# Kernel optimization log

Hardware: AMD Instinct MI355X
Metric: run time of the kernel (lower is better)

Reference implementation:

```python
import jax, jax.numpy as jnp
import numpy as np

B, SQ, SK = 2, 2048, 2048
QDIM = KDIM = HID = 1024
H = 16
DH = HID // H  # inner_dim = 64


def setup_inputs() -> dict:
    key = jax.random.key(0)
    ks = jax.random.split(key, 8)
    q = jax.random.normal(ks[0], (B, SQ, QDIM), dtype=jnp.float32)
    k = jax.random.normal(ks[1], (B, SK, KDIM), dtype=jnp.float32)
    v = jax.random.normal(ks[2], (B, SK, KDIM), dtype=jnp.float32)
    mask = jax.random.randint(ks[3], (B, SQ, SK), 0, 2).astype(jnp.bool_)
    scale = 1.0 / np.sqrt(QDIM)
    # per-head projections, stored stacked: [H, in_dim, DH]
    Wq = jax.random.normal(ks[4], (H, QDIM, DH), dtype=jnp.float32) * scale
    Wk = jax.random.normal(ks[5], (H, KDIM, DH), dtype=jnp.float32) * scale
    Wv = jax.random.normal(ks[6], (H, KDIM, DH), dtype=jnp.float32) * scale
    Wo = jax.random.normal(ks[7], (HID, QDIM), dtype=jnp.float32) * scale
    return {"q": q, "k": k, "v": v, "mask": mask,
            "Wq": Wq, "Wk": Wk, "Wv": Wv, "Wo": Wo}


def reference(q, k, v, mask, Wq, Wk, Wv, Wo):
    dh = Wq.shape[-1]
    qh = jnp.einsum('bsd,hde->bhse', q, Wq)   # [B,H,SQ,DH]
    kh = jnp.einsum('bsd,hde->bhse', k, Wk)   # [B,H,SK,DH]
    vh = jnp.einsum('bsd,hde->bhse', v, Wv)   # [B,H,SK,DH]
    scores = jnp.einsum('bhqd,bhkd->bhqk', qh, kh) / jnp.sqrt(jnp.asarray(dh, qh.dtype))
    scores = jnp.where(mask[:, None, :, :], -jnp.inf, scores)
    attn = jax.nn.softmax(scores, axis=-1)
    att = jnp.einsum('bhqk,bhkd->bhqd', attn, vh)        # [B,H,SQ,DH]
    concat = att.transpose(0, 2, 1, 3).reshape(q.shape[0], q.shape[1], -1)  # head-order concat
    return concat @ Wo  # [B,SQ,QDIM]
```

## Files before the change

### kernel.cpp

```cpp
#include <hip/hip_runtime.h>

#define NB 2
#define NH 16
#define SEQ 2048
#define DMODEL 1024
#define DHEAD 64
#define QSCALE 0.18033688f

typedef __attribute__((ext_vector_type(8))) short bf16x8;
typedef __attribute__((ext_vector_type(4))) short bf16x4;
typedef __attribute__((ext_vector_type(4))) float f32x4;
typedef __attribute__((ext_vector_type(16))) float f32x16;
typedef __attribute__((ext_vector_type(4))) int i32x4;

static __device__ __forceinline__ unsigned short f2bf(float f) {
    unsigned int u = __float_as_uint(f);
    u += 0x7fffu + ((u >> 16) & 1u);
    return (unsigned short)(u >> 16);
}
static __device__ __forceinline__ unsigned int pk2(float lo, float hi) {
    return (unsigned int)f2bf(lo) | ((unsigned int)f2bf(hi) << 16);
}
static __device__ __forceinline__ void gld_lds16(const unsigned short* g, unsigned short* l) {
    __builtin_amdgcn_global_load_lds(
        (const __attribute__((address_space(1))) unsigned int*)g,
        (__attribute__((address_space(3))) unsigned int*)l, 16, 0, 0);
}

__global__ __launch_bounds__(256) void prep_kernel(
    const int* __restrict__ mask, unsigned long long* __restrict__ mpack,
    const float* __restrict__ Wq, const float* __restrict__ Wk, const float* __restrict__ Wv,
    unsigned short* __restrict__ Wqt, unsigned short* __restrict__ Wkt,
    unsigned short* __restrict__ Wvt,
    const float* __restrict__ Wo, unsigned short* __restrict__ Wot)
{
    __shared__ __align__(16) float Ls[64][65];
    const int bid = blockIdx.x, t = threadIdx.x;

    if (bid < 1024) {
        const int wave = bid * 4 + (t >> 6);
        const int lane = t & 63;
        const int* row = mask + (size_t)wave * SEQ;
        unsigned long long* orow = mpack + (size_t)wave * (SEQ / 64);
        for (int w = 0; w < SEQ / 64; ++w) {
            int m = row[w * 64 + lane];
            unsigned long long bits = __ballot(m != 0);
            if (lane == 0) orow[w] = bits;
        }
    } else {
        const float* S; unsigned short* D; float scale; int R, tile_r, tile_c, ostride;
        if (bid < 1792) {
            const int local = bid - 1024, z = local >> 4, sel = z >> 4, h = z & 15;
            S = (sel == 0 ? Wq : sel == 1 ? Wk : Wv) + (size_t)h * DMODEL * DHEAD;
            D = (sel == 0 ? Wqt : sel == 1 ? Wkt : Wvt) + (size_t)h * DMODEL * DHEAD;
            scale = (sel == 0) ? QSCALE : 1.0f;
            tile_r = (local & 15) * 64; tile_c = 0; R = DHEAD; ostride = DMODEL;
        } else {
            const int local = bid - 1792;
            S = Wo; D = Wot; scale = 1.0f;
            tile_c = (local & 15) * 64; tile_r = (local >> 4) * 64; R = DMODEL; ostride = DMODEL;
        }
        const int c4 = (t & 15) * 4;
        for (int rr = t >> 4; rr < 64; rr += 16) {
            float4 x = *(const float4*)(S + (size_t)(tile_r + rr) * R + tile_c + c4);
            Ls[rr][c4 + 0] = x.x; Ls[rr][c4 + 1] = x.y;
            Ls[rr][c4 + 2] = x.z; Ls[rr][c4 + 3] = x.w;
        }
        __syncthreads();
        const int r4 = (t & 15) * 4;
        for (int cc = t >> 4; cc < 64; cc += 16) {
            ushort4 o;
            o.x = f2bf(Ls[r4 + 0][cc] * scale); o.y = f2bf(Ls[r4 + 1][cc] * scale);
            o.z = f2bf(Ls[r4 + 2][cc] * scale); o.w = f2bf(Ls[r4 + 3][cc] * scale);
            *(ushort4*)(D + (size_t)(tile_c + cc) * ostride + tile_r + r4) = o;
        }
    }
}

__global__ __launch_bounds__(256) void proj_gemm_kernel(
    const float* __restrict__ qf32, const float* __restrict__ kf32,
    const float* __restrict__ vf32,
    const unsigned short* __restrict__ Wqt, const unsigned short* __restrict__ Wkt,
    const unsigned short* __restrict__ Wvt,
    unsigned short* __restrict__ qh, unsigned short* __restrict__ kh,
    unsigned short* __restrict__ vt)
{
    const int bid = blockIdx.x;
    const int sx = bid >> 3;
    const int mtg = (bid & 7) * 12 + (sx >> 3);
    const int z = mtg >> 5;
    const int m0 = (mtg & 31) * 128;
    const int n0 = (sx & 7) * 128;

    const float* Af = (z == 0) ? qf32 : (z == 1) ? kf32 : vf32;
    const unsigned short* Bt = (z == 0) ? Wqt : (z == 1) ? Wkt : Wvt;

    const int t = threadIdx.x, lane = t & 63, w = t >> 6;
    const int lg = lane >> 4, ln = lane & 15;
    const int wx = w & 1, wy = w >> 1;

    __shared__ __align__(16) unsigned short SM[32768];

    int an[4], ac[4];
    #pragma unroll
    for (int i = 0; i < 4; ++i) {
        const int s = i * 256 + t;
        an[i] = s >> 3;
        ac[i] = (s & 7) ^ (an[i] & 7);
    }

    f32x4 acc[4][4] = {};
    float4 ast[4][2];

    #pragma unroll
    for (int i = 0; i < 4; ++i) {
        const float* src = Af + (size_t)(m0 + an[i]) * DMODEL + ac[i] * 8;
        ast[i][0] = *(const float4*)(src);
        ast[i][1] = *(const float4*)(src + 4);
    }
    #pragma unroll
    for (int i = 0; i < 4; ++i) {
        int s = (w * 4 + i) * 64 + lane;
        int n = s >> 3, c = (s & 7) ^ (n & 7);
        gld_lds16(Bt + (size_t)(n0 + n) * DMODEL + c * 8, SM + 16384 + (size_t)s * 8);
    }
    #pragma unroll
    for (int i = 0; i < 4; ++i) {
        uint4 val;
        val.x = pk2(ast[i][0].x, ast[i][0].y); val.y = pk2(ast[i][0].z, ast[i][0].w);
        val.z = pk2(ast[i][1].x, ast[i][1].y); val.w = pk2(ast[i][1].z, ast[i][1].w);
        *(uint4*)(SM + (size_t)(i * 256 + t) * 8) = val;
    }
    __syncthreads();

    for (int ki = 0; ki < 16; ++ki) {
        const int buf = ki & 1;

        if (ki < 15) {
            const int kk = (ki + 1) * 64;
            #pragma unroll
            for (int i = 0; i < 4; ++i) {
                const float* src = Af + (size_t)(m0 + an[i]) * DMODEL + kk + ac[i] * 8;
                ast[i][0] = *(const float4*)(src);
                ast[i][1] = *(const float4*)(src + 4);
            }
            #pragma unroll
            for (int i = 0; i < 4; ++i) {
                int s = (w * 4 + i) * 64 + lane;
                int n = s >> 3, c = (s & 7) ^ (n & 7);
                gld_lds16(Bt + (size_t)(n0 + n) * DMODEL + kk + c * 8,
                          SM + 16384 + (buf ^ 1) * 8192 + (size_t)s * 8);
            }
        }

        const unsigned short* Asb = SM + buf * 8192;
        const unsigned short* Bsb = SM + 16384 + buf * 8192;
        #pragma unroll
        for (int ks = 0; ks < 2; ++ks) {
            bf16x8 af[4], bf[4];
            #pragma unroll
            for (int rb = 0; rb < 4; ++rb) {
                int r = wy * 64 + rb * 16 + ln;
                af[rb] = *(const bf16x8*)(Asb + r * 64 + (((ks * 4 + lg) ^ (r & 7)) * 8));
            }
            #pragma unroll
            for (int nb = 0; nb < 4; ++nb) {
                int n = wx * 64 + nb * 16 + ln;
                bf[nb] = *(const bf16x8*)(Bsb + n * 64 + (((ks * 4 + lg) ^ (n & 7)) * 8));
            }
            #pragma unroll
            for (int rb = 0; rb < 4; ++rb)
                #pragma unroll
                for (int nb = 0; nb < 4; ++nb)
                    acc[rb][nb] = __builtin_amdgcn_mfma_f32_16x16x32_bf16(
                        af[rb], bf[nb], acc[rb][nb], 0, 0, 0);
        }

        if (ki < 15) {
            unsigned short* Ad = SM + (buf ^ 1) * 8192;
            #pragma unroll
            for (int i = 0; i < 4; ++i) {
                uint4 val;
                val.x = pk2(ast[i][0].x, ast[i][0].y); val.y = pk2(ast[i][0].z, ast[i][0].w);
                val.z = pk2(ast[i][1].x, ast[i][1].y); val.w = pk2(ast[i][1].z, ast[i][1].w);
                *(uint4*)(Ad + (size_t)(i * 256 + t) * 8) = val;
            }
        }
        __syncthreads();
    }

    if (z < 2) {
        unsigned short* Y = (z == 0) ? qh : kh;
        unsigned short* Ep = SM;
        #pragma unroll
        for (int rb = 0; rb < 4; ++rb)
            #pragma unroll
            for (int nb = 0; nb < 4; ++nb) {
                const int c_l = wx * 64 + nb * 16 + ln;
                const int base = ((c_l >> 6) << 13) + (c_l & 63);
                #pragma unroll
                for (int r = 0; r < 4; ++r) {
                    const int s_l = wy * 64 + rb * 16 + lg * 4 + r;
                    Ep[base + s_l * 64] = f2bf(acc[rb][nb][r]);
                }
            }
        __syncthreads();
        {
            const int head = t >> 7, r2 = t & 127;
            const unsigned short* src = Ep + head * 8192 + r2 * 64;
            unsigned short* dst = Y + ((size_t)((m0 >> 11) * NH + (n0 >> 6) + head) * SEQ
                                       + (m0 & (SEQ - 1)) + r2) * DHEAD;
            #pragma unroll
            for (int i = 0; i < 8; ++i)
                *(uint4*)(dst + i * 8) = *(const uint4*)(src + i * 8);
        }
    } else {
        unsigned short* Ep = SM;
        #pragma unroll
        for (int rb = 0; rb < 4; ++rb)
            #pragma unroll
            for (int nb = 0; nb < 4; ++nb) {
                const int c_l = wx * 64 + nb * 16 + ln;
                const int seq0 = wy * 64 + rb * 16 + lg * 4;
                ushort4 o;
                o.x = f2bf(acc[rb][nb][0]); o.y = f2bf(acc[rb][nb][1]);
                o.z = f2bf(acc[rb][nb][2]); o.w = f2bf(acc[rb][nb][3]);
                *(ushort4*)(Ep + (c_l >> 6) * 8704 + (c_l & 63) * 136 + seq0) = o;
            }
        __syncthreads();
        {
            const int head = t >> 7, dh = (t >> 1) & 63, hf = t & 1;
            const unsigned short* src = Ep + head * 8704 + dh * 136 + hf * 64;
            unsigned short* dst = vt
                + ((size_t)((((m0 >> 11) << 4) + (n0 >> 6) + head) * DHEAD + dh) * SEQ
                   + (m0 & (SEQ - 1)) + hf * 64);
            #pragma unroll
            for (int i = 0; i < 8; ++i)
                *(uint4*)(dst + i * 8) = *(const uint4*)(src + i * 8);
        }
    }
}

__global__ __launch_bounds__(512, 4) void attn_kernel(
    const unsigned short* __restrict__ qh, const unsigned short* __restrict__ kh,
    const unsigned short* __restrict__ vt, const unsigned long long* __restrict__ mpack,
    unsigned short* __restrict__ att)
{
    const int t = threadIdx.x, lane = t & 63;
    const int w8 = t >> 6;
    const int half = w8 >> 2, w = w8 & 3;
    const int th = t & 255;
    const int h = lane >> 5, lq = lane & 31;
    const int L = lq & 7, X = (lq >> 3) & 3;

    const int bid = blockIdx.x;
    const int r_ = bid >> 3;
    const int qt = r_ & 15;
    const int bh = (bid & 7) * 4 + (r_ >> 4);
    const int b = bh >> 4, hd = bh & 15;
    const int row0 = qt * 128;
    const int qrow = row0 + w * 32 + lq;
    const int kt0 = half * (SEQ / 2);

    __shared__ __align__(16) unsigned short SMEM[2 * 16384];
    unsigned short* Kh = SMEM + half * 16384;
    unsigned short* Vh = Kh + 8192;

    const unsigned short* Kb = kh + (size_t)bh * SEQ * DHEAD;
    const unsigned short* Vb = vt + (size_t)bh * DHEAD * SEQ;

    const unsigned short* Qb = qh + ((size_t)bh * SEQ + qrow) * DHEAD;
    bf16x8 qf[4];
    #pragma unroll
    for (int d = 0; d < 4; ++d) qf[d] = *(const bf16x8*)(Qb + d * 16 + h * 8);

    const unsigned long long* Mb = mpack + ((size_t)b * SEQ + qrow) * (SEQ / 64);

    int oK[2], oV[2], sL[2];
    #pragma unroll
    for (int i = 0; i < 2; ++i) {
        const int s = i * 256 + th;
        const int n = s >> 3, c = (s & 7) ^ (n & 7) ^ ((n >> 3) & 3);
        sL[i] = s * 8;
        oK[i] = n * DHEAD + c * 8;
        oV[i] = n * SEQ + c * 8;
    }

    f32x16 acc[2] = {};
    f32x16 lacc = {};
    bf16x8 ones;
    #pragma unroll
    for (int i = 0; i < 8; ++i) ones[i] = (short)0x3f80;

    unsigned long long mw, mwn = 0;

    #pragma unroll
    for (int i = 0; i < 2; ++i)
        gld_lds16(Kb + (size_t)kt0 * DHEAD + oK[i], Kh + sL[i]);
    #pragma unroll
    for (int i = 0; i < 2; ++i)
        gld_lds16(Vb + (size_t)kt0 + oV[i], Vh + sL[i]);
    mw = Mb[half << 4];
    __syncthreads();

    for (int tix = 0; tix < 16; ++tix) {
        const int buf = tix & 1;

        if (tix < 15) {
            const int ktn = kt0 + (tix + 1) * 64;
            unsigned short* Kd = Kh + (buf ^ 1) * 4096;
            unsigned short* Vd = Vh + (buf ^ 1) * 4096;
            #pragma unroll
            for (int i = 0; i < 2; ++i)
                gld_lds16(Kb + (size_t)ktn * DHEAD + oK[i], Kd + sL[i]);
            #pragma unroll
            for (int i = 0; i < 2; ++i)
                gld_lds16(Vb + (size_t)ktn + oV[i], Vd + sL[i]);
            mwn = Mb[(half << 4) + tix + 1];
        }

        const unsigned short* Ksb = Kh + buf * 4096;
        const unsigned short* Vsb = Vh + buf * 4096;
        const unsigned long long mh_ = mw >> (h * 4);

        #pragma unroll
        for (int st = 0; st < 2; ++st) {
            f32x16 S = {};
            __builtin_amdgcn_s_setprio(1);
            #pragma unroll
            for (int d = 0; d < 4; ++d) {
                bf16x8 kf = *(const bf16x8*)(Ksb + (st * 32 + lq) * 64
                                             + (((d * 2 + h) ^ L ^ X) * 8));
                S = __builtin_amdgcn_mfma_f32_32x32x16_bf16(kf, qf[d], S, 0, 0, 0);
            }
            __builtin_amdgcn_s_setprio(0);
            const unsigned int wn = ~(unsigned int)(mh_ >> (32 * st));
            unsigned int pd[8];
            #pragma unroll
            for (int bb = 0; bb < 4; ++bb) {
                float e[4];
                #pragma unroll
                for (int rr = 0; rr < 4; ++rr) {
                    const int keep = __builtin_amdgcn_sbfe(wn, 8 * bb + rr, 1);
                    float ex = __builtin_amdgcn_exp2f(S[bb * 4 + rr]);
                    e[rr] = __uint_as_float(__float_as_uint(ex) & (unsigned int)keep);
                }
                pd[bb * 2 + 0] = __builtin_amdgcn_perm(
                    __float_as_uint(e[1]), __float_as_uint(e[0]), 0x07060302u);
                pd[bb * 2 + 1] = __builtin_amdgcn_perm(
                    __float_as_uint(e[3]), __float_as_uint(e[2]), 0x07060302u);
            }
            #pragma unroll
            for (int k2 = 0; k2 < 2; ++k2) {
                i32x4 pi = { (int)pd[4 * k2 + 0], (int)pd[4 * k2 + 1],
                             (int)pd[4 * k2 + 2], (int)pd[4 * k2 + 3] };
                bf16x8 pf = __builtin_bit_cast(bf16x8, pi);
                const int p0 = (((4 * st + 2 * k2) ^ L ^ X)) * 8;
                bf16x8 vf0, vf1;
                {
                    const unsigned short* vb_ = Vsb + lq * 64 + 4 * h;
                    bf16x4 a0 = *(const bf16x4*)(vb_ + p0);
                    bf16x4 a1 = *(const bf16x4*)(vb_ + (p0 ^ 8));
                    vf0 = __builtin_shufflevector(a0, a1, 0, 1, 2, 3, 4, 5, 6, 7);
                    const unsigned short* vc_ = vb_ + 32 * 64;
                    bf16x4 c0 = *(const bf16x4*)(vc_ + p0);
                    bf16x4 c1 = *(const bf16x4*)(vc_ + (p0 ^ 8));
                    vf1 = __builtin_shufflevector(c0, c1, 0, 1, 2, 3, 4, 5, 6, 7);
                }
                __builtin_amdgcn_s_setprio(1);
                lacc = __builtin_amdgcn_mfma_f32_32x32x16_bf16(ones, pf, lacc, 0, 0, 0);
                acc[0] = __builtin_amdgcn_mfma_f32_32x32x16_bf16(vf0, pf, acc[0], 0, 0, 0);
                acc[1] = __builtin_amdgcn_mfma_f32_32x32x16_bf16(vf1, pf, acc[1], 0, 0, 0);
                __builtin_amdgcn_s_setprio(0);
            }
        }

        mw = mwn;
        __syncthreads();
    }

    const int rloc = w * 32 + lq;
    float* Osh = (float*)SMEM;
    float* Lsh = (float*)SMEM + 128 * 68;

    if (half == 1) {
        #pragma unroll
        for (int dt = 0; dt < 2; ++dt)
            #pragma unroll
            for (int g = 0; g < 4; ++g) {
                f32x4 v = { acc[dt][g * 4 + 0], acc[dt][g * 4 + 1],
                            acc[dt][g * 4 + 2], acc[dt][g * 4 + 3] };
                *(f32x4*)(Osh + rloc * 68 + dt * 32 + 8 * g + 4 * h) = v;
            }
        if (h == 0) Lsh[rloc] = lacc[0];
    }
    __syncthreads();
    if (half == 0) {
        const float linv = 1.0f / (lacc[0] + Lsh[rloc]);
        unsigned short* Ar = att + ((size_t)b * SEQ + qrow) * DMODEL + hd * DHEAD;
        #pragma unroll
        for (int dt = 0; dt < 2; ++dt)
            #pragma unroll
            for (int g = 0; g < 4; ++g) {
                const int dh0 = dt * 32 + 8 * g + 4 * h;
                f32x4 p = *(const f32x4*)(Osh + rloc * 68 + dh0);
                ushort4 o;
                o.x = f2bf((acc[dt][g * 4 + 0] + p[0]) * linv);
                o.y = f2bf((acc[dt][g * 4 + 1] + p[1]) * linv);
                o.z = f2bf((acc[dt][g * 4 + 2] + p[2]) * linv);
                o.w = f2bf((acc[dt][g * 4 + 3] + p[3]) * linv);
                *(ushort4*)(Ar + dh0) = o;
            }
    }
}

__global__ __launch_bounds__(256) void out_gemm_kernel(
    const unsigned short* __restrict__ A, const unsigned short* __restrict__ Bt,
    float* __restrict__ C)
{
    const int bid = blockIdx.x;
    const int sx = bid >> 3;
    const int m0 = ((bid & 7) * 8 + (sx >> 3)) * 64;
    const int n0 = (sx & 7) * 128;

    const int t = threadIdx.x, lane = t & 63, w = t >> 6;
    const int lg = lane >> 4, ln = lane & 15;
    const int wx = w & 1, wy = w >> 1;

    __shared__ __align__(16) unsigned short SM[24576];

    f32x4 acc[2][4] = {};

    {
        unsigned short* Ad = SM;
        unsigned short* Bd = SM + 8192;
        #pragma unroll
        for (int i = 0; i < 4; ++i) {
            int s = (w * 4 + i) * 64 + lane;
            int n = s >> 3, c = (s & 7) ^ (n & 7);
            gld_lds16(Bt + (size_t)(n0 + n) * DMODEL + c * 8, Bd + (size_t)s * 8);
        }
        #pragma unroll
        for (int i = 0; i < 2; ++i) {
            int s = (w * 2 + i) * 64 + lane;
            int n = s >> 3, c = (s & 7) ^ (n & 7);
            gld_lds16(A + (size_t)(m0 + n) * DMODEL + c * 8, Ad + (size_t)s * 8);
        }
    }
    __syncthreads();

    for (int ki = 0; ki < 16; ++ki) {
        const int buf = ki & 1;

        if (ki < 15) {
            const int kk = (ki + 1) * 64;
            unsigned short* Ad = SM + (buf ^ 1) * 4096;
            unsigned short* Bd = SM + 8192 + (buf ^ 1) * 8192;
            #pragma unroll
            for (int i = 0; i < 4; ++i) {
                int s = (w * 4 + i) * 64 + lane;
                int n = s >> 3, c = (s & 7) ^ (n & 7);
                gld_lds16(Bt + (size_t)(n0 + n) * DMODEL + kk + c * 8, Bd + (size_t)s * 8);
            }
            #pragma unroll
            for (int i = 0; i < 2; ++i) {
                int s = (w * 2 + i) * 64 + lane;
                int n = s >> 3, c = (s & 7) ^ (n & 7);
                gld_lds16(A + (size_t)(m0 + n) * DMODEL + kk + c * 8, Ad + (size_t)s * 8);
            }
        }

        const unsigned short* Asb = SM + buf * 4096;
        const unsigned short* Bsb = SM + 8192 + buf * 8192;
        #pragma unroll
        for (int ks = 0; ks < 2; ++ks) {
            bf16x8 af[2], bf[4];
            #pragma unroll
            for (int rb = 0; rb < 2; ++rb) {
                int rr = wy * 32 + rb * 16 + ln;
                af[rb] = *(const bf16x8*)(Asb + rr * 64 + (((ks * 4 + lg) ^ (rr & 7)) * 8));
            }
            #pragma unroll
            for (int nb = 0; nb < 4; ++nb) {
                int n = wx * 64 + nb * 16 + ln;
                bf[nb] = *(const bf16x8*)(Bsb + n * 64 + (((ks * 4 + lg) ^ (n & 7)) * 8));
            }
            #pragma unroll
            for (int rb = 0; rb < 2; ++rb)
                #pragma unroll
                for (int nb = 0; nb < 4; ++nb)
                    acc[rb][nb] = __builtin_amdgcn_mfma_f32_16x16x32_bf16(
                        af[rb], bf[nb], acc[rb][nb], 0, 0, 0);
        }
        __syncthreads();
    }

    #pragma unroll
    for (int rb = 0; rb < 2; ++rb)
        #pragma unroll
        for (int nb = 0; nb < 4; ++nb)
            #pragma unroll
            for (int rr = 0; rr < 4; ++rr) {
                int grow = m0 + wy * 32 + rb * 16 + lg * 4 + rr;
                int gcol = n0 + wx * 64 + nb * 16 + ln;
                C[(size_t)grow * DMODEL + gcol] = acc[rb][nb][rr];
            }
}

extern "C" void kernel_launch(void* const* d_in, const int* in_sizes, int n_in,
                              void* d_out, int out_size, void* d_ws, size_t ws_size,
                              hipStream_t stream) {
    const float* q    = (const float*)d_in[0];
    const float* k    = (const float*)d_in[1];
    const float* v    = (const float*)d_in[2];
    const int*   mask = (const int*)  d_in[3];
    const float* Wq   = (const float*)d_in[4];
    const float* Wk   = (const float*)d_in[5];
    const float* Wv   = (const float*)d_in[6];
    const float* Wo   = (const float*)d_in[7];
    float* out = (float*)d_out;

    unsigned short* ws  = (unsigned short*)d_ws;
    const size_t n1 = (size_t)NB * NH * SEQ * DHEAD;
    const size_t nw = (size_t)NH * DHEAD * DMODEL;
    unsigned short* qh  = ws;
    unsigned short* kh  = qh + n1;
    unsigned short* vt  = kh + n1;
    unsigned short* att = vt + n1;
    unsigned short* Wqt = att + n1;
    unsigned short* Wkt = Wqt + nw;
    unsigned short* Wvt = Wkt + nw;
    unsigned short* Wot = Wvt + nw;
    unsigned long long* mpack = (unsigned long long*)(Wot + nw);

    prep_kernel<<<dim3(2048), 256, 0, stream>>>(
        mask, mpack, Wq, Wk, Wv, Wqt, Wkt, Wvt, Wo, Wot);
    proj_gemm_kernel<<<dim3(768), 256, 0, stream>>>(q, k, v, Wqt, Wkt, Wvt, qh, kh, vt);
    attn_kernel<<<dim3(512), 512, 0, stream>>>(qh, kh, vt, mpack, att);
    out_gemm_kernel<<<dim3(512), 256, 0, stream>>>(att, Wot, out);
}
```

Measured before the change: 278.3 us.

## Pre-convert q/k/v to bf16 in prep kernel and use async LDS loads in projection GEMM

The prep kernel gains 6144 extra blocks that convert the fp32 q, k and v activations to bf16 in workspace buffers. The projection GEMM then loads its A tiles with global_load_lds straight into shared memory, the same way it loads the weights. This removes the register staging, in-loop packing and LDS stores from the GEMM main loop. In exchange it adds an extra pass that reads all q/k/v and writes bf16 copies, plus more workspace, and it assumes the workspace is large enough for the new buffers.

```diff
diff --git a/kernel.cpp b/kernel.cpp
--- a/kernel.cpp
+++ b/kernel.cpp
@@ -32,7 +32,10 @@
     const float* __restrict__ Wq, const float* __restrict__ Wk, const float* __restrict__ Wv,
     unsigned short* __restrict__ Wqt, unsigned short* __restrict__ Wkt,
     unsigned short* __restrict__ Wvt,
-    const float* __restrict__ Wo, unsigned short* __restrict__ Wot)
+    const float* __restrict__ Wo, unsigned short* __restrict__ Wot,
+    const float* __restrict__ q, const float* __restrict__ k, const float* __restrict__ v,
+    unsigned short* __restrict__ qb, unsigned short* __restrict__ kb,
+    unsigned short* __restrict__ vb)
 {
     __shared__ __align__(16) float Ls[64][65];
     const int bid = blockIdx.x, t = threadIdx.x;
@@ -47,7 +50,7 @@
             unsigned long long bits = __ballot(m != 0);
             if (lane == 0) orow[w] = bits;
         }
-    } else {
+    } else if (bid < 2048) {
         const float* S; unsigned short* D; float scale; int R, tile_r, tile_c, ostride;
         if (bid < 1792) {
             const int local = bid - 1024, z = local >> 4, sel = z >> 4, h = z & 15;
@@ -74,12 +77,24 @@
             o.z = f2bf(Ls[r4 + 2][cc] * scale); o.w = f2bf(Ls[r4 + 3][cc] * scale);
             *(ushort4*)(D + (size_t)(tile_c + cc) * ostride + tile_r + r4) = o;
         }
+    } else {
+        const int local = bid - 2048;
+        const int z = local >> 11;
+        const float* S = (z == 0) ? q : (z == 1) ? k : v;
+        unsigned short* D = (z == 0) ? qb : (z == 1) ? kb : vb;
+        const size_t i = ((size_t)(local & 2047) * 256 + t) * 8;
+        float4 x0 = *(const float4*)(S + i);
+        float4 x1 = *(const float4*)(S + i + 4);
+        uint4 val;
+        val.x = pk2(x0.x, x0.y); val.y = pk2(x0.z, x0.w);
+        val.z = pk2(x1.x, x1.y); val.w = pk2(x1.z, x1.w);
+        *(uint4*)(D + i) = val;
     }
 }
 
 __global__ __launch_bounds__(256) void proj_gemm_kernel(
-    const float* __restrict__ qf32, const float* __restrict__ kf32,
-    const float* __restrict__ vf32,
+    const unsigned short* __restrict__ qb, const unsigned short* __restrict__ kb,
+    const unsigned short* __restrict__ vb,
     const unsigned short* __restrict__ Wqt, const unsigned short* __restrict__ Wkt,
     const unsigned short* __restrict__ Wvt,
     unsigned short* __restrict__ qh, unsigned short* __restrict__ kh,
@@ -92,7 +107,7 @@
     const int m0 = (mtg & 31) * 128;
     const int n0 = (sx & 7) * 128;
 
-    const float* Af = (z == 0) ? qf32 : (z == 1) ? kf32 : vf32;
+    const unsigned short* A  = (z == 0) ? qb : (z == 1) ? kb : vb;
     const unsigned short* Bt = (z == 0) ? Wqt : (z == 1) ? Wkt : Wvt;
 
     const int t = threadIdx.x, lane = t & 63, w = t >> 6;
@@ -101,36 +116,20 @@
 
     __shared__ __align__(16) unsigned short SM[32768];
 
-    int an[4], ac[4];
+    f32x4 acc[4][4] = {};
+
     #pragma unroll
     for (int i = 0; i < 4; ++i) {
-        const int s = i * 256 + t;
-        an[i] = s >> 3;
-        ac[i] = (s & 7) ^ (an[i] & 7);
-    }
-
-    f32x4 acc[4][4] = {};
-    float4 ast[4][2];
-
+        int s = i * 256 + t;
+        int n = s >> 3, c = (s & 7) ^ (n & 7);
+        gld_lds16(A + (size_t)(m0 + n) * DMODEL + c * 8, SM + (size_t)s * 8);
+    }
     #pragma unroll
     for (int i = 0; i < 4; ++i) {
-        const float* src = Af + (size_t)(m0 + an[i]) * DMODEL + ac[i] * 8;
-        ast[i][0] = *(const float4*)(src);
-        ast[i][1] = *(const float4*)(src + 4);
-    }
-    #pragma unroll
-    for (int i = 0; i < 4; ++i) {
-        int s = (w * 4 + i) * 64 + lane;
+        int s = i * 256 + t;
         int n = s >> 3, c = (s & 7) ^ (n & 7);
         gld_lds16(Bt + (size_t)(n0 + n) * DMODEL + c * 8, SM + 16384 + (size_t)s * 8);
     }
-    #pragma unroll
-    for (int i = 0; i < 4; ++i) {
-        uint4 val;
-        val.x = pk2(ast[i][0].x, ast[i][0].y); val.y = pk2(ast[i][0].z, ast[i][0].w);
-        val.z = pk2(ast[i][1].x, ast[i][1].y); val.w = pk2(ast[i][1].z, ast[i][1].w);
-        *(uint4*)(SM + (size_t)(i * 256 + t) * 8) = val;
-    }
     __syncthreads();
 
     for (int ki = 0; ki < 16; ++ki) {
@@ -138,18 +137,19 @@
 
         if (ki < 15) {
             const int kk = (ki + 1) * 64;
+            unsigned short* Ad = SM + (buf ^ 1) * 8192;
+            unsigned short* Bd = SM + 16384 + (buf ^ 1) * 8192;
             #pragma unroll
             for (int i = 0; i < 4; ++i) {
-                const float* src = Af + (size_t)(m0 + an[i]) * DMODEL + kk + ac[i] * 8;
-                ast[i][0] = *(const float4*)(src);
-                ast[i][1] = *(const float4*)(src + 4);
+                int s = i * 256 + t;
+                int n = s >> 3, c = (s & 7) ^ (n & 7);
+                gld_lds16(A + (size_t)(m0 + n) * DMODEL + kk + c * 8, Ad + (size_t)s * 8);
             }
             #pragma unroll
             for (int i = 0; i < 4; ++i) {
-                int s = (w * 4 + i) * 64 + lane;
+                int s = i * 256 + t;
                 int n = s >> 3, c = (s & 7) ^ (n & 7);
-                gld_lds16(Bt + (size_t)(n0 + n) * DMODEL + kk + c * 8,
-                          SM + 16384 + (buf ^ 1) * 8192 + (size_t)s * 8);
+                gld_lds16(Bt + (size_t)(n0 + n) * DMODEL + kk + c * 8, Bd + (size_t)s * 8);
             }
         }
 
@@ -174,17 +174,6 @@
                 for (int nb = 0; nb < 4; ++nb)
                     acc[rb][nb] = __builtin_amdgcn_mfma_f32_16x16x32_bf16(
                         af[rb], bf[nb], acc[rb][nb], 0, 0, 0);
-        }
-
-        if (ki < 15) {
-            unsigned short* Ad = SM + (buf ^ 1) * 8192;
-            #pragma unroll
-            for (int i = 0; i < 4; ++i) {
-                uint4 val;
-                val.x = pk2(ast[i][0].x, ast[i][0].y); val.y = pk2(ast[i][0].z, ast[i][0].w);
-                val.z = pk2(ast[i][1].x, ast[i][1].y); val.w = pk2(ast[i][1].z, ast[i][1].w);
-                *(uint4*)(Ad + (size_t)(i * 256 + t) * 8) = val;
-            }
         }
         __syncthreads();
     }
@@ -532,10 +521,13 @@
     unsigned short* Wvt = Wkt + nw;
     unsigned short* Wot = Wvt + nw;
     unsigned long long* mpack = (unsigned long long*)(Wot + nw);
-
-    prep_kernel<<<dim3(2048), 256, 0, stream>>>(
-        mask, mpack, Wq, Wk, Wv, Wqt, Wkt, Wvt, Wo, Wot);
-    proj_gemm_kernel<<<dim3(768), 256, 0, stream>>>(q, k, v, Wqt, Wkt, Wvt, qh, kh, vt);
+    unsigned short* qb = (unsigned short*)(mpack + (size_t)NB * SEQ * (SEQ / 64));
+    unsigned short* kb = qb + n1;
+    unsigned short* vb = kb + n1;
+
+    prep_kernel<<<dim3(8192), 256, 0, stream>>>(
+        mask, mpack, Wq, Wk, Wv, Wqt, Wkt, Wvt, Wo, Wot, q, k, v, qb, kb, vb);
+    proj_gemm_kernel<<<dim3(768), 256, 0, stream>>>(qb, kb, vb, Wqt, Wkt, Wvt, qh, kh, vt);
     attn_kernel<<<dim3(512), 512, 0, stream>>>(qh, kh, vt, mpack, att);
     out_gemm_kernel<<<dim3(512), 256, 0, stream>>>(att, Wot, out);
 }
```

New measurement: 248.2 us. 10.8% less time.
